# Optimization experiments

Measured on AMD Instinct MI355X. Metric: run time of the kernel, lower is better.

The kernel has to match this reference:

```python
import jax, jax.numpy as jnp
import numpy as np
from functools import partial


def deform_sample(inp, dy, dx):
    """Bilinear sample inp[b,c] at (y+dy[b,c,y,x], x+dx[b,c,y,x]) with zero padding.
    inp, dy, dx: [B, C, H, W] -> [B, C, H, W]. Matches torchvision deform_conv2d
    with 1x1 kernel and offset_groups == C (one offset pair per channel)."""
    B, C, H, W = inp.shape
    ys = jnp.arange(H, dtype=inp.dtype)[None, None, :, None] + dy  # [B,C,H,W]
    xs = jnp.arange(W, dtype=inp.dtype)[None, None, None, :] + dx
    y0f = jnp.floor(ys)
    x0f = jnp.floor(xs)
    wy = ys - y0f
    wx = xs - x0f
    y0 = y0f.astype(jnp.int32)
    x0 = x0f.astype(jnp.int32)
    flat = inp.reshape(B, C, H * W)

    def gather(yi, xi):
        valid = (yi >= 0) & (yi < H) & (xi >= 0) & (xi < W)
        idx = jnp.clip(yi, 0, H - 1) * W + jnp.clip(xi, 0, W - 1)
        v = jnp.take_along_axis(flat, idx.reshape(B, C, H * W), axis=2).reshape(B, C, H, W)
        return jnp.where(valid, v, jnp.zeros((), inp.dtype))

    return ((1 - wy) * (1 - wx) * gather(y0, x0)
            + (1 - wy) * wx * gather(y0, x0 + 1)
            + wy * (1 - wx) * gather(y0 + 1, x0)
            + wy * wx * gather(y0 + 1, x0 + 1))


def atm_layer(x, offset, w_weight, w_bias, h_weight, h_bias, local_weight, local_bias,
              fc1_w, fc1_b, fc2_w, fc2_b, proj_w, proj_b):
    B, H, W, C = x.shape
    x_nchw = jnp.transpose(x, (0, 3, 1, 2))  # [B,C,H,W]
    zeros = jnp.zeros_like(x_nchw)

    # ATM along w: offset[:, :C] is x-offset (offset_t[:,1::2]), y-offset 0
    sw = deform_sample(x_nchw, zeros, offset[:, :C])
    w = jnp.einsum('bchw,oc->bhwo', sw, w_weight) + w_bias  # [B,H,W,C]

    # ATM along h: offset[:, C:] is y-offset (offset_t[:,0::2]), x-offset 0
    sh = deform_sample(x_nchw, offset[:, C:], zeros)
    h = jnp.einsum('bchw,oc->bhwo', sh, h_weight) + h_bias

    # depthwise 5x5 conv, padding 2
    c = jax.lax.conv_general_dilated(
        x_nchw, local_weight, window_strides=(1, 1), padding=((2, 2), (2, 2)),
        feature_group_count=C, dimension_numbers=('NCHW', 'OIHW', 'NCHW'))
    c = jnp.transpose(c, (0, 2, 3, 1)) + local_bias  # [B,H,W,C]

    # gating MLP: global average -> fc1 -> GELU -> fc2 -> softmax over 3 branches
    a = (w + h + c).mean(axis=(1, 2))  # [B,C]
    a = jax.nn.gelu(a @ fc1_w.T + fc1_b, approximate=False)
    a = a @ fc2_w.T + fc2_b  # [B,3C]
    a = jnp.transpose(a.reshape(B, C, 3), (2, 0, 1))  # [3,B,C]
    a = jax.nn.softmax(a, axis=0)[:, :, None, None, :]  # [3,B,1,1,C]

    out = w * a[0] + h * a[1] + c * a[2]
    out = out @ proj_w.T + proj_b
    return out


def setup_inputs() -> dict:
    C = 256
    B, H, W = 16, 64, 64
    key = jax.random.key(0)
    ks = jax.random.split(key, 16)
    bnd = 1.0 / np.sqrt(C)
    hid = C // 4
    return {
        'x': jax.random.normal(ks[0], (B, H, W, C), jnp.float32),
        'offset': jax.random.normal(ks[1], (B, 2 * C, H, W), jnp.float32),
        'w_weight': jax.random.uniform(ks[2], (C, C), jnp.float32, -bnd, bnd),
        'w_bias': jax.random.uniform(ks[3], (C,), jnp.float32, -bnd, bnd),
        'h_weight': jax.random.uniform(ks[4], (C, C), jnp.float32, -bnd, bnd),
        'h_bias': jax.random.uniform(ks[5], (C,), jnp.float32, -bnd, bnd),
        'local_weight': jax.random.uniform(ks[6], (C, 1, 5, 5), jnp.float32, -0.2, 0.2),
        'local_bias': jax.random.uniform(ks[7], (C,), jnp.float32, -0.2, 0.2),
        'fc1_w': jax.random.uniform(ks[8], (hid, C), jnp.float32, -bnd, bnd),
        'fc1_b': jax.random.uniform(ks[9], (hid,), jnp.float32, -bnd, bnd),
        'fc2_w': jax.random.uniform(ks[10], (3 * C, hid), jnp.float32, -1.0 / np.sqrt(hid), 1.0 / np.sqrt(hid)),
        'fc2_b': jax.random.uniform(ks[11], (3 * C,), jnp.float32, -1.0 / np.sqrt(hid), 1.0 / np.sqrt(hid)),
        'proj_w': jax.random.uniform(ks[12], (C, C), jnp.float32, -bnd, bnd),
        'proj_b': jax.random.uniform(ks[13], (C,), jnp.float32, -bnd, bnd),
    }


def reference(x, offset, w_weight, w_bias, h_weight, h_bias, local_weight, local_bias,
              fc1_w, fc1_b, fc2_w, fc2_b, proj_w, proj_b):
    return atm_layer(x, offset, w_weight, w_bias, h_weight, h_bias, local_weight,
                     local_bias, fc1_w, fc1_b, fc2_w, fc2_b, proj_w, proj_b)
```

## Files before the change

kernel.cpp:

```cpp
#include <hip/hip_runtime.h>
#include <hip/hip_bf16.h>

typedef _Float16 half4_t __attribute__((ext_vector_type(4)));
typedef _Float16 half8 __attribute__((ext_vector_type(8)));
typedef float f32x4 __attribute__((ext_vector_type(4)));

#define BB 16
#define HH 64
#define WW2 64
#define CC 256

__global__ __launch_bounds__(256) void k_pre(
    const float* __restrict__ Ww, const float* __restrict__ Wh,
    const float* __restrict__ pw,
    _Float16* __restrict__ WwT, _Float16* __restrict__ WhT,
    _Float16* __restrict__ pf, float* __restrict__ sums)
{
  __shared__ _Float16 tile[64][65];
  const int blk = blockIdx.x;
  const int t = threadIdx.x;

  if (blk < 32) {
    const int nt = blk & 3, kt = (blk >> 2) & 3, mat = blk >> 4;
    const float* src = mat ? Wh : Ww;
    _Float16* dst = mat ? WhT : WwT;
    const int n0 = nt * 64, k0 = kt * 64;
    const int sl = t & 63;
    #pragma unroll
    for (int p = 0; p < 16; p++) {
      int chl = (t >> 6) + p * 4;
      tile[chl][sl] = (_Float16)src[(size_t)(n0 + chl) * 256 + k0 + sl];
    }
    __syncthreads();
    #pragma unroll
    for (int p = 0; p < 2; p++) {
      int pl = (t >> 3) + p * 32;
      int c8 = (t & 7) * 8;
      half8 hv;
      #pragma unroll
      for (int r = 0; r < 8; r++) hv[r] = tile[c8 + r][pl];
      *(half8*)(dst + (size_t)(k0 + pl) * 256 + n0 + c8) = hv;
    }
  } else if (blk < 80) {
    sums[(blk - 32) * 256 + t] = 0.f;
  } else {
    int i = (blk - 80) * 2048 + t * 8;
    float4 v0 = *(const float4*)(pw + i);
    float4 v1 = *(const float4*)(pw + i + 4);
    half8 h = {(_Float16)v0.x, (_Float16)v0.y, (_Float16)v0.z, (_Float16)v0.w,
               (_Float16)v1.x, (_Float16)v1.y, (_Float16)v1.z, (_Float16)v1.w};
    *(half8*)(pf + i) = h;
  }
}

__global__ __launch_bounds__(256) void k_transA(
    const float* __restrict__ x, const float* __restrict__ off,
    _Float16* __restrict__ swb, float* __restrict__ ssw)
{
  __shared__ _Float16 tile[64][65];
  __shared__ _Float16 xr[64][68];
  __shared__ float red[4][64];

  const int work = (blockIdx.x & 7) * 512 + (blockIdx.x >> 3);
  const int st   = work & 63;
  const int cht  = (work >> 6) & 3;
  const int b    = work >> 8;
  const int t = threadIdx.x;

  const int ch0 = cht * 64;
  const float* src = off + ((size_t)b * 512 + ch0) * 4096 + st * 64;
  const int sl = t & 63;
  #pragma unroll
  for (int p = 0; p < 16; p++) {
    int chl = (t >> 6) + p * 4;
    tile[chl][sl] = (_Float16)src[(size_t)chl * 4096 + sl];
  }

  const float* xs_src = x + ((size_t)(b * 64 + st) * 64) * 256 + ch0;
  const int xrow = t >> 2;
  const int c16 = (t & 3) * 16;
  #pragma unroll
  for (int j = 0; j < 4; j++) {
    float4 v = *(const float4*)(xs_src + (size_t)xrow * 256 + c16 + j * 4);
    half4_t h = {(_Float16)v.x, (_Float16)v.y, (_Float16)v.z, (_Float16)v.w};
    *(half4_t*)(&xr[xrow][c16 + j * 4]) = h;
  }
  __syncthreads();

  const int cl = t & 63, xg = t >> 6;
  const int cg = ch0 + cl;
  _Float16* sp = swb + ((size_t)(b * 64 + st) * 64) * 256 + cg;
  float asw = 0.f;
  #pragma unroll
  for (int k = 0; k < 16; k++) {
    int xi = xg * 16 + k;
    float dx = (float)tile[cl][xi];
    float xs2 = (float)xi + dx;
    float xf = floorf(xs2);
    float wx = xs2 - xf;
    int xq = (int)xf;
    float v0 = (xq >= 0 && xq < 64) ? (float)xr[xq][cl] : 0.f;
    float v1 = (xq + 1 >= 0 && xq + 1 < 64) ? (float)xr[xq + 1][cl] : 0.f;
    float swv = (1.f - wx) * v0 + wx * v1;
    sp[(size_t)xi * 256] = (_Float16)swv;
    asw += swv;
  }
  red[xg][cl] = asw;
  __syncthreads();
  if (t < 64)
    atomicAdd(&ssw[b * CC + ch0 + t],
              red[0][t] + red[1][t] + red[2][t] + red[3][t]);
}

__global__ __launch_bounds__(256) void k_transB(const float* __restrict__ off,
                                                _Float16* __restrict__ offBT)
{
  __shared__ _Float16 tile[64][65];
  const int work = (blockIdx.x & 7) * 512 + (blockIdx.x >> 3);
  const int st   = work & 63;
  const int cht  = (work >> 6) & 3;
  const int b    = work >> 8;
  const int t = threadIdx.x;

  const int ch0 = 256 + cht * 64;
  const float* src = off + ((size_t)b * 512 + ch0) * 4096 + st * 64;
  const int sl = t & 63;
  #pragma unroll
  for (int p = 0; p < 16; p++) {
    int chl = (t >> 6) + p * 4;
    tile[chl][sl] = (_Float16)src[(size_t)chl * 4096 + sl];
  }
  __syncthreads();

  #pragma unroll
  for (int p = 0; p < 2; p++) {
    int pl = (t >> 3) + p * 32;
    int c8 = (t & 7) * 8;
    half8 hv;
    #pragma unroll
    for (int r = 0; r < 8; r++) hv[r] = tile[c8 + r][pl];
    int s = st * 64 + pl;
    size_t pix = (size_t)b * 4096 + (s & 63) * 64 + (s >> 6);
    *(half8*)(offBT + pix * 256 + cht * 64 + c8) = hv;
  }
}

__global__ __launch_bounds__(256) void k_conv(
    const float* __restrict__ x, const float* __restrict__ lw,
    _Float16* __restrict__ cvb, float* __restrict__ scv)
{
  const int work = (blockIdx.x & 7) * 128 + (blockIdx.x >> 3);
  const int b = work >> 6, y = work & 63;
  const int c = threadIdx.x;

  float wgt[25];
  #pragma unroll
  for (int q = 0; q < 25; q++) wgt[q] = lw[c * 25 + q];

  const float* xb = x + (size_t)b * HH * WW2 * CC + c;
  const float* rp[5];
  bool yv[5];
  #pragma unroll
  for (int ky = 0; ky < 5; ky++) {
    int yy = y + ky - 2;
    yv[ky] = (yy >= 0 && yy < HH);
    rp[ky] = xb + (size_t)(yv[ky] ? yy : 0) * WW2 * CC;
  }

  _Float16* cp = cvb + ((size_t)b * 4096 + y * 64) * CC + c;
  float acc5[5] = {0.f, 0.f, 0.f, 0.f, 0.f};
  float acv = 0.f;

  #pragma unroll 5
  for (int u = 0; u < 70; ++u) {
    acc5[(u + 2) % 5] = 0.f;
    if (u < 64) {
      float c0 = yv[0] ? rp[0][u * CC] : 0.f;
      float c1 = yv[1] ? rp[1][u * CC] : 0.f;
      float c2 = yv[2] ? rp[2][u * CC] : 0.f;
      float c3 = yv[3] ? rp[3][u * CC] : 0.f;
      float c4 = yv[4] ? rp[4][u * CC] : 0.f;
      #pragma unroll
      for (int kx = 0; kx < 5; kx++) {
        acc5[(u + 7 - kx) % 5] += wgt[0 + kx] * c0 + wgt[5 + kx] * c1 +
                                  wgt[10 + kx] * c2 + wgt[15 + kx] * c3 +
                                  wgt[20 + kx] * c4;
      }
    }
    int xi = u - 2;
    if (xi >= 0 && xi < 64) {
      float cv = acc5[(u + 3) % 5];
      cp[(size_t)xi * CC] = (_Float16)cv;
      acv += cv;
    }
  }
  atomicAdd(&scv[b * CC + c], acv);
}

__global__ __launch_bounds__(256) void k_col(
    const float* __restrict__ x, const _Float16* __restrict__ offBT,
    _Float16* __restrict__ shb, float* __restrict__ ssh)
{
  __shared__ _Float16 xc[HH * CC];
  const int work = (blockIdx.x & 7) * 128 + (blockIdx.x >> 3);
  const int b = work >> 6, xi = work & 63;
  const int t = threadIdx.x;
  const int c = t;

  #pragma unroll
  for (int p = 0; p < 16; p++) {
    int yy = p * 4 + (t >> 6);
    int c4 = (t & 63) * 4;
    float4 v = *(const float4*)(x + ((size_t)(b * HH + yy) * WW2 + xi) * CC + c4);
    half4_t h = {(_Float16)v.x, (_Float16)v.y, (_Float16)v.z, (_Float16)v.w};
    *(half4_t*)(xc + yy * CC + c4) = h;
  }
  __syncthreads();

  const _Float16* obt = offBT + ((size_t)(b * WW2 + xi) * HH) * CC + c;
  _Float16* hp = shb + ((size_t)(b * HH) * WW2 + xi) * CC + c;
  float ash = 0.f;
  #pragma unroll 8
  for (int yy = 0; yy < 64; yy++) {
    float dy = (float)obt[(size_t)yy * CC];
    float ys = (float)yy + dy;
    float yf = floorf(ys);
    float wy = ys - yf;
    int yq = (int)yf;
    float u0 = (yq >= 0 && yq < HH) ? (float)xc[yq * CC + c] : 0.f;
    float u1 = (yq + 1 >= 0 && yq + 1 < HH) ? (float)xc[(yq + 1) * CC + c] : 0.f;
    float shv = (1.f - wy) * u0 + wy * u1;
    hp[(size_t)yy * WW2 * CC] = (_Float16)shv;
    ash += shv;
  }
  atomicAdd(&ssh[b * CC + c], ash);
}

__global__ __launch_bounds__(256) void k_gate(
    const float* __restrict__ ssw, const float* __restrict__ ssh, const float* __restrict__ scv,
    const float* __restrict__ Ww, const float* __restrict__ bw,
    const float* __restrict__ Wh, const float* __restrict__ bh,
    const float* __restrict__ blc,
    const float* __restrict__ fc1w, const float* __restrict__ fc1b,
    const float* __restrict__ fc2w, const float* __restrict__ fc2b,
    _Float16* __restrict__ gh, float* __restrict__ bcomb)
{
  __shared__ float sswl[CC], sshl[CC], avgl[CC], tl[64];
  const int b = blockIdx.x, tid = threadIdx.x;
  sswl[tid] = ssw[b * CC + tid];
  sshl[tid] = ssh[b * CC + tid];
  __syncthreads();

  float acc = scv[b * CC + tid];
  for (int c = 0; c < CC; c++)
    acc += sswl[c] * Ww[tid * CC + c] + sshl[c] * Wh[tid * CC + c];
  avgl[tid] = acc * (1.f / (HH * WW2)) + bw[tid] + bh[tid] + blc[tid];
  __syncthreads();

  if (tid < 64) {
    float a = fc1b[tid];
    for (int o = 0; o < CC; o++) a += avgl[o] * fc1w[tid * CC + o];
    tl[tid] = 0.5f * a * (1.f + erff(a * 0.70710678118654752f));
  }
  __syncthreads();

  float g[3];
  #pragma unroll
  for (int j = 0; j < 3; j++) {
    float a = fc2b[tid * 3 + j];
    for (int k = 0; k < 64; k++) a += tl[k] * fc2w[(tid * 3 + j) * 64 + k];
    g[j] = a;
  }
  float m = fmaxf(g[0], fmaxf(g[1], g[2]));
  float e0 = expf(g[0] - m), e1 = expf(g[1] - m), e2 = expf(g[2] - m);
  float inv = 1.f / (e0 + e1 + e2);
  float a0 = e0 * inv, a1 = e1 * inv, a2 = e2 * inv;
  gh[(0 * BB + b) * CC + tid] = (_Float16)a0;
  gh[(1 * BB + b) * CC + tid] = (_Float16)a1;
  gh[(2 * BB + b) * CC + tid] = (_Float16)a2;
  bcomb[b * CC + tid] = a0 * bw[tid] + a1 * bh[tid] + a2 * blc[tid];
}

__global__ __launch_bounds__(256) void k_mats(
    const _Float16* __restrict__ pf, const _Float16* __restrict__ gh,
    const _Float16* __restrict__ WwT, const _Float16* __restrict__ WhT,
    const float* __restrict__ bcomb, const float* __restrict__ pb,
    _Float16* __restrict__ Bcat, float* __restrict__ bias_out)
{
  const int blk = (blockIdx.x & 7) * 16 + (blockIdx.x >> 3);
  const int ob = blk & 3;
  const int br = (blk >> 2) & 1;
  const int b  = blk >> 3;
  const int o0 = ob * 64;
  const int tid = threadIdx.x;
  const int wid = tid >> 6, l = tid & 63;
  const int n0 = wid * 64;
  const int lr = l & 15;
  const int kg = (l >> 4) * 8;
  const int jr = (l >> 4) * 4;

  const _Float16* WT  = br ? WhT : WwT;
  const _Float16* ghb = gh + (size_t)(br * BB + b) * CC;

  f32x4 acc[4][4];
  #pragma unroll
  for (int mi = 0; mi < 4; mi++)
    #pragma unroll
    for (int ni = 0; ni < 4; ni++) acc[mi][ni] = (f32x4){0.f, 0.f, 0.f, 0.f};

  #pragma unroll
  for (int ks = 0; ks < 8; ks++) {
    half8 gv = *(const half8*)(ghb + kg + ks * 32);
    half8 a[4], bbv[4];
    #pragma unroll
    for (int mi = 0; mi < 4; mi++)
      a[mi] = *(const half8*)(pf + (size_t)(o0 + mi * 16 + lr) * CC + kg + ks * 32) * gv;
    #pragma unroll
    for (int ni = 0; ni < 4; ni++)
      bbv[ni] = *(const half8*)(WT + (size_t)(n0 + ni * 16 + lr) * CC + kg + ks * 32);
    #pragma unroll
    for (int mi = 0; mi < 4; mi++)
      #pragma unroll
      for (int ni = 0; ni < 4; ni++)
        acc[mi][ni] = __builtin_amdgcn_mfma_f32_16x16x32_f16(a[mi], bbv[ni], acc[mi][ni], 0, 0, 0);
  }

  #pragma unroll
  for (int ni = 0; ni < 4; ni++) {
    int kcol = n0 + ni * 16 + lr;
    #pragma unroll
    for (int mi = 0; mi < 4; mi++) {
      #pragma unroll
      for (int j = 0; j < 4; j++) {
        int o = o0 + mi * 16 + jr + j;
        Bcat[((size_t)b * CC + o) * 512 + br * 256 + kcol] = (_Float16)acc[mi][ni][j];
      }
    }
  }

  if (br == 0) {
    int o_l = tid >> 2, part = tid & 3;
    const _Float16* pr = pf + (size_t)(o0 + o_l) * CC + part * 64;
    const float* bc = bcomb + b * CC + part * 64;
    float s = 0.f;
    #pragma unroll
    for (int i = 0; i < 8; i++) {
      half8 h = *(const half8*)(pr + i * 8);
      #pragma unroll
      for (int r = 0; r < 8; r++) s += (float)h[r] * bc[i * 8 + r];
    }
    s += __shfl_xor(s, 1);
    s += __shfl_xor(s, 2);
    if (part == 0) bias_out[b * CC + o0 + o_l] = s + pb[o0 + o_l];
  }
}

#define APAD 264
__global__ __launch_bounds__(256) void k_gemm(
    const _Float16* __restrict__ swb, const _Float16* __restrict__ shb,
    const _Float16* __restrict__ cvb, const _Float16* __restrict__ Bcat,
    const _Float16* __restrict__ pf, const _Float16* __restrict__ a2h,
    const float* __restrict__ bias_out, float* __restrict__ out)
{
  __shared__ _Float16 smem[64 * APAD];

  const int work = (blockIdx.x & 7) * 128 + (blockIdx.x >> 3);
  const int r0 = work * 64;
  const int b = work >> 6;
  const int tid = threadIdx.x;
  const int wid = tid >> 6, l = tid & 63;
  const int n0 = wid * 64;
  const int lr = l & 15;
  const int kg = (l >> 4) * 8;
  const int jr = (l >> 4) * 4;

  const _Float16* bq = Bcat + ((size_t)b * CC + n0 + lr) * 512 + kg;

  f32x4 acc[4][4];
  #pragma unroll
  for (int mi = 0; mi < 4; mi++)
    #pragma unroll
    for (int ni = 0; ni < 4; ni++) acc[mi][ni] = (f32x4){0.f, 0.f, 0.f, 0.f};

  half8 st[8];
  {
    const _Float16* g = swb + (size_t)r0 * CC;
    #pragma unroll
    for (int p = 0; p < 8; p++) st[p] = *(const half8*)(g + p * 2048 + tid * 8);
    #pragma unroll
    for (int p = 0; p < 8; p++) {
      int i = p * 2048 + tid * 8;
      *(half8*)(smem + (i >> 8) * APAD + (i & 255)) = st[p];
    }
  }
  __syncthreads();
  {
    const _Float16* g = shb + (size_t)r0 * CC;
    #pragma unroll
    for (int p = 0; p < 8; p++) st[p] = *(const half8*)(g + p * 2048 + tid * 8);
  }
  #pragma unroll
  for (int ks = 0; ks < 8; ks++) {
    half8 a[4], bbv[4];
    #pragma unroll
    for (int mi = 0; mi < 4; mi++)
      a[mi] = *(const half8*)(smem + (mi * 16 + lr) * APAD + kg + ks * 32);
    #pragma unroll
    for (int ni = 0; ni < 4; ni++)
      bbv[ni] = *(const half8*)(bq + (size_t)ni * 16 * 512 + ks * 32);
    #pragma unroll
    for (int mi = 0; mi < 4; mi++)
      #pragma unroll
      for (int ni = 0; ni < 4; ni++)
        acc[mi][ni] = __builtin_amdgcn_mfma_f32_16x16x32_f16(a[mi], bbv[ni], acc[mi][ni], 0, 0, 0);
  }
  __syncthreads();
  #pragma unroll
  for (int p = 0; p < 8; p++) {
    int i = p * 2048 + tid * 8;
    *(half8*)(smem + (i >> 8) * APAD + (i & 255)) = st[p];
  }
  __syncthreads();
  {
    const _Float16* g = cvb + (size_t)r0 * CC;
    #pragma unroll
    for (int p = 0; p < 8; p++) st[p] = *(const half8*)(g + p * 2048 + tid * 8);
  }
  #pragma unroll
  for (int ks = 0; ks < 8; ks++) {
    half8 a[4], bbv[4];
    #pragma unroll
    for (int mi = 0; mi < 4; mi++)
      a[mi] = *(const half8*)(smem + (mi * 16 + lr) * APAD + kg + ks * 32);
    #pragma unroll
    for (int ni = 0; ni < 4; ni++)
      bbv[ni] = *(const half8*)(bq + (size_t)ni * 16 * 512 + 256 + ks * 32);
    #pragma unroll
    for (int mi = 0; mi < 4; mi++)
      #pragma unroll
      for (int ni = 0; ni < 4; ni++)
        acc[mi][ni] = __builtin_amdgcn_mfma_f32_16x16x32_f16(a[mi], bbv[ni], acc[mi][ni], 0, 0, 0);
  }
  __syncthreads();
  #pragma unroll
  for (int p = 0; p < 8; p++) {
    int i = p * 2048 + tid * 8;
    *(half8*)(smem + (i >> 8) * APAD + (i & 255)) = st[p];
  }
  __syncthreads();
  const _Float16* a2b = a2h + (size_t)b * CC;
  #pragma unroll
  for (int ks = 0; ks < 8; ks++) {
    half8 a2v = *(const half8*)(a2b + kg + ks * 32);
    half8 a[4], bbv[4];
    #pragma unroll
    for (int mi = 0; mi < 4; mi++)
      a[mi] = *(const half8*)(smem + (mi * 16 + lr) * APAD + kg + ks * 32);
    #pragma unroll
    for (int ni = 0; ni < 4; ni++)
      bbv[ni] = *(const half8*)(pf + (size_t)(n0 + ni * 16 + lr) * CC + kg + ks * 32) * a2v;
    #pragma unroll
    for (int mi = 0; mi < 4; mi++)
      #pragma unroll
      for (int ni = 0; ni < 4; ni++)
        acc[mi][ni] = __builtin_amdgcn_mfma_f32_16x16x32_f16(a[mi], bbv[ni], acc[mi][ni], 0, 0, 0);
  }

  #pragma unroll
  for (int ni = 0; ni < 4; ni++) {
    int col = n0 + ni * 16 + lr;
    float bo = bias_out[b * CC + col];
    #pragma unroll
    for (int mi = 0; mi < 4; mi++) {
      #pragma unroll
      for (int j = 0; j < 4; j++) {
        size_t idx = (size_t)(r0 + mi * 16 + jr + j) * CC + col;
        out[idx] = acc[mi][ni][j] + bo;
      }
    }
  }
}

extern "C" void kernel_launch(void* const* d_in, const int* in_sizes, int n_in,
                              void* d_out, int out_size, void* d_ws, size_t ws_size,
                              hipStream_t stream)
{
  const float* x    = (const float*)d_in[0];
  const float* off  = (const float*)d_in[1];
  const float* Ww   = (const float*)d_in[2];
  const float* bw   = (const float*)d_in[3];
  const float* Wh   = (const float*)d_in[4];
  const float* bh   = (const float*)d_in[5];
  const float* lw   = (const float*)d_in[6];
  const float* blc  = (const float*)d_in[7];
  const float* fc1w = (const float*)d_in[8];
  const float* fc1b = (const float*)d_in[9];
  const float* fc2w = (const float*)d_in[10];
  const float* fc2b = (const float*)d_in[11];
  const float* pw   = (const float*)d_in[12];
  const float* pb   = (const float*)d_in[13];
  float* out = (float*)d_out;

  char* ws = (char*)d_ws;
  _Float16* shb   = (_Float16*)(ws + 0);
  _Float16* cvb   = (_Float16*)(ws + 33554432);
  _Float16* offBT = (_Float16*)(ws + 67108864);
  _Float16* swb   = (_Float16*)(ws + 100663296);
  _Float16* Bcat  = (_Float16*)(ws + 134217728);
  _Float16* pf    = (_Float16*)(ws + 138412032);
  _Float16* gh    = (_Float16*)(ws + 138543104);
  float* bcomb    = (float*)(ws + 138567680);
  float* bias_out = (float*)(ws + 138584064);
  _Float16* WwT = (_Float16*)((char*)d_out + 0);
  _Float16* WhT = (_Float16*)((char*)d_out + 131072);
  float* sums   = (float*)((char*)d_out + 262144);
  float* ssw = sums, *ssh = sums + 4096, *scv = sums + 8192;

  k_pre<<<112, 256, 0, stream>>>(Ww, Wh, pw, WwT, WhT, pf, sums);
  k_transB<<<4096, 256, 0, stream>>>(off, offBT);
  k_col<<<BB * WW2, 256, 0, stream>>>(x, offBT, shb, ssh);
  k_transA<<<4096, 256, 0, stream>>>(x, off, swb, ssw);
  k_conv<<<BB * HH, 256, 0, stream>>>(x, lw, cvb, scv);
  k_gate<<<BB, 256, 0, stream>>>(ssw, ssh, scv, Ww, bw, Wh, bh, blc,
                                 fc1w, fc1b, fc2w, fc2b, gh, bcomb);
  k_mats<<<128, 256, 0, stream>>>(pf, gh, WwT, WhT, bcomb, pb, Bcat, bias_out);
  k_gemm<<<1024, 256, 0, stream>>>(swb, shb, cvb, Bcat, pf, gh + 2 * BB * CC,
                                   bias_out, out);
}
```

Baseline: 261.1 us.

## Split conv, column-sample and GEMM kernels into finer blocks for more parallelism

Doubles the grid for k_conv, k_col and k_gemm by halving each block's work. k_conv now splits each row into x-halves and computes 8 outputs per group from a 12-column register window instead of a rolling accumulator. k_col splits channels in half, so each block stages only 128 channels in LDS and two thread groups cover 32 rows each. k_gemm moves from 64-row to 32-row tiles. The aim is better occupancy and load balance across the CUs (1024 blocks is only a few waves). The cost is redundant halo loads in the conv, more atomics, and more reloads of the B matrix in the GEMM.

```diff
diff --git a/kernel.cpp b/kernel.cpp
--- a/kernel.cpp
+++ b/kernel.cpp
@@ -149,8 +149,10 @@
     const float* __restrict__ x, const float* __restrict__ lw,
     _Float16* __restrict__ cvb, float* __restrict__ scv)
 {
-  const int work = (blockIdx.x & 7) * 128 + (blockIdx.x >> 3);
-  const int b = work >> 6, y = work & 63;
+  const int work = (blockIdx.x & 7) * 256 + (blockIdx.x >> 3);
+  const int xh = work & 1;
+  const int y  = (work >> 1) & 63;
+  const int b  = work >> 7;
   const int c = threadIdx.x;
 
   float wgt[25];
@@ -168,29 +170,34 @@
   }
 
   _Float16* cp = cvb + ((size_t)b * 4096 + y * 64) * CC + c;
-  float acc5[5] = {0.f, 0.f, 0.f, 0.f, 0.f};
   float acv = 0.f;
-
-  #pragma unroll 5
-  for (int u = 0; u < 70; ++u) {
-    acc5[(u + 2) % 5] = 0.f;
-    if (u < 64) {
-      float c0 = yv[0] ? rp[0][u * CC] : 0.f;
-      float c1 = yv[1] ? rp[1][u * CC] : 0.f;
-      float c2 = yv[2] ? rp[2][u * CC] : 0.f;
-      float c3 = yv[3] ? rp[3][u * CC] : 0.f;
-      float c4 = yv[4] ? rp[4][u * CC] : 0.f;
+  const int x0 = xh * 32;
+
+  for (int g = 0; g < 4; ++g) {
+    const int u0 = x0 + g * 8;
+    float col[60];
+    #pragma unroll
+    for (int j = 0; j < 12; j++) {
+      int xx = u0 + j - 2;
+      bool xv = (xx >= 0 && xx < 64);
+      int xxc = xv ? xx : 0;
+      #pragma unroll
+      for (int ky = 0; ky < 5; ky++) {
+        float v = rp[ky][(size_t)xxc * CC];
+        col[j * 5 + ky] = (xv && yv[ky]) ? v : 0.f;
+      }
+    }
+    #pragma unroll
+    for (int o = 0; o < 8; o++) {
+      float cv = 0.f;
       #pragma unroll
       for (int kx = 0; kx < 5; kx++) {
-        acc5[(u + 7 - kx) % 5] += wgt[0 + kx] * c0 + wgt[5 + kx] * c1 +
-                                  wgt[10 + kx] * c2 + wgt[15 + kx] * c3 +
-                                  wgt[20 + kx] * c4;
+        const int j5 = (o + kx) * 5;
+        cv += wgt[0 + kx]  * col[j5 + 0] + wgt[5 + kx]  * col[j5 + 1] +
+              wgt[10 + kx] * col[j5 + 2] + wgt[15 + kx] * col[j5 + 3] +
+              wgt[20 + kx] * col[j5 + 4];
       }
-    }
-    int xi = u - 2;
-    if (xi >= 0 && xi < 64) {
-      float cv = acc5[(u + 3) % 5];
-      cp[(size_t)xi * CC] = (_Float16)cv;
+      cp[(size_t)(u0 + o) * CC] = (_Float16)cv;
       acv += cv;
     }
   }
@@ -201,39 +208,46 @@
     const float* __restrict__ x, const _Float16* __restrict__ offBT,
     _Float16* __restrict__ shb, float* __restrict__ ssh)
 {
-  __shared__ _Float16 xc[HH * CC];
-  const int work = (blockIdx.x & 7) * 128 + (blockIdx.x >> 3);
-  const int b = work >> 6, xi = work & 63;
+  __shared__ _Float16 xc[64 * 128];
+  const int work = (blockIdx.x & 7) * 256 + (blockIdx.x >> 3);
+  const int ch = work & 1;
+  const int xi = (work >> 1) & 63;
+  const int b  = work >> 7;
+  const int ch0 = ch * 128;
   const int t = threadIdx.x;
-  const int c = t;
-
-  #pragma unroll
-  for (int p = 0; p < 16; p++) {
-    int yy = p * 4 + (t >> 6);
-    int c4 = (t & 63) * 4;
-    float4 v = *(const float4*)(x + ((size_t)(b * HH + yy) * WW2 + xi) * CC + c4);
-    half4_t h = {(_Float16)v.x, (_Float16)v.y, (_Float16)v.z, (_Float16)v.w};
-    *(half4_t*)(xc + yy * CC + c4) = h;
-  }
-  __syncthreads();
-
-  const _Float16* obt = offBT + ((size_t)(b * WW2 + xi) * HH) * CC + c;
-  _Float16* hp = shb + ((size_t)(b * HH) * WW2 + xi) * CC + c;
+
+  #pragma unroll
+  for (int p = 0; p < 4; p++) {
+    int i = p * 2048 + t * 8;
+    int yy = i >> 7, cl = i & 127;
+    const float* s = x + ((size_t)(b * 64 + yy) * 64 + xi) * 256 + ch0 + cl;
+    float4 v0 = *(const float4*)(s);
+    float4 v1 = *(const float4*)(s + 4);
+    half8 h = {(_Float16)v0.x, (_Float16)v0.y, (_Float16)v0.z, (_Float16)v0.w,
+               (_Float16)v1.x, (_Float16)v1.y, (_Float16)v1.z, (_Float16)v1.w};
+    *(half8*)(xc + i) = h;
+  }
+  __syncthreads();
+
+  const int cl = t & 127, yg = t >> 7;
+  const _Float16* obt = offBT + ((size_t)(b * 64 + xi) * 64) * 256 + ch0 + cl;
+  _Float16* hp = shb + ((size_t)(b * 64) * 64 + xi) * 256 + ch0 + cl;
   float ash = 0.f;
   #pragma unroll 8
-  for (int yy = 0; yy < 64; yy++) {
-    float dy = (float)obt[(size_t)yy * CC];
+  for (int k = 0; k < 32; k++) {
+    int yy = yg * 32 + k;
+    float dy = (float)obt[(size_t)yy * 256];
     float ys = (float)yy + dy;
     float yf = floorf(ys);
     float wy = ys - yf;
     int yq = (int)yf;
-    float u0 = (yq >= 0 && yq < HH) ? (float)xc[yq * CC + c] : 0.f;
-    float u1 = (yq + 1 >= 0 && yq + 1 < HH) ? (float)xc[(yq + 1) * CC + c] : 0.f;
+    float u0 = (yq >= 0 && yq < 64) ? (float)xc[yq * 128 + cl] : 0.f;
+    float u1 = (yq + 1 >= 0 && yq + 1 < 64) ? (float)xc[(yq + 1) * 128 + cl] : 0.f;
     float shv = (1.f - wy) * u0 + wy * u1;
-    hp[(size_t)yy * WW2 * CC] = (_Float16)shv;
+    hp[(size_t)yy * 64 * 256] = (_Float16)shv;
     ash += shv;
   }
-  atomicAdd(&ssh[b * CC + c], ash);
+  atomicAdd(&ssh[b * CC + ch0 + cl], ash);
 }
 
 __global__ __launch_bounds__(256) void k_gate(
@@ -362,11 +376,11 @@
     const _Float16* __restrict__ pf, const _Float16* __restrict__ a2h,
     const float* __restrict__ bias_out, float* __restrict__ out)
 {
-  __shared__ _Float16 smem[64 * APAD];
-
-  const int work = (blockIdx.x & 7) * 128 + (blockIdx.x >> 3);
-  const int r0 = work * 64;
-  const int b = work >> 6;
+  __shared__ _Float16 smem[32 * APAD];
+
+  const int work = (blockIdx.x & 7) * 256 + (blockIdx.x >> 3);
+  const int r0 = work * 32;
+  const int b = work >> 7;
   const int tid = threadIdx.x;
   const int wid = tid >> 6, l = tid & 63;
   const int n0 = wid * 64;
@@ -376,19 +390,19 @@
 
   const _Float16* bq = Bcat + ((size_t)b * CC + n0 + lr) * 512 + kg;
 
-  f32x4 acc[4][4];
-  #pragma unroll
-  for (int mi = 0; mi < 4; mi++)
+  f32x4 acc[2][4];
+  #pragma unroll
+  for (int mi = 0; mi < 2; mi++)
     #pragma unroll
     for (int ni = 0; ni < 4; ni++) acc[mi][ni] = (f32x4){0.f, 0.f, 0.f, 0.f};
 
-  half8 st[8];
+  half8 st[4];
   {
     const _Float16* g = swb + (size_t)r0 * CC;
     #pragma unroll
-    for (int p = 0; p < 8; p++) st[p] = *(const half8*)(g + p * 2048 + tid * 8);
-    #pragma unroll
-    for (int p = 0; p < 8; p++) {
+    for (int p = 0; p < 4; p++) st[p] = *(const half8*)(g + p * 2048 + tid * 8);
+    #pragma unroll
+    for (int p = 0; p < 4; p++) {
       int i = p * 2048 + tid * 8;
       *(half8*)(smem + (i >> 8) * APAD + (i & 255)) = st[p];
     }
@@ -397,26 +411,26 @@
   {
     const _Float16* g = shb + (size_t)r0 * CC;
     #pragma unroll
-    for (int p = 0; p < 8; p++) st[p] = *(const half8*)(g + p * 2048 + tid * 8);
+    for (int p = 0; p < 4; p++) st[p] = *(const half8*)(g + p * 2048 + tid * 8);
   }
   #pragma unroll
   for (int ks = 0; ks < 8; ks++) {
-    half8 a[4], bbv[4];
-    #pragma unroll
-    for (int mi = 0; mi < 4; mi++)
+    half8 a[2], bbv[4];
+    #pragma unroll
+    for (int mi = 0; mi < 2; mi++)
       a[mi] = *(const half8*)(smem + (mi * 16 + lr) * APAD + kg + ks * 32);
     #pragma unroll
     for (int ni = 0; ni < 4; ni++)
       bbv[ni] = *(const half8*)(bq + (size_t)ni * 16 * 512 + ks * 32);
     #pragma unroll
-    for (int mi = 0; mi < 4; mi++)
+    for (int mi = 0; mi < 2; mi++)
       #pragma unroll
       for (int ni = 0; ni < 4; ni++)
         acc[mi][ni] = __builtin_amdgcn_mfma_f32_16x16x32_f16(a[mi], bbv[ni], acc[mi][ni], 0, 0, 0);
   }
   __syncthreads();
   #pragma unroll
-  for (int p = 0; p < 8; p++) {
+  for (int p = 0; p < 4; p++) {
     int i = p * 2048 + tid * 8;
     *(half8*)(smem + (i >> 8) * APAD + (i & 255)) = st[p];
   }
@@ -424,26 +438,26 @@
   {
     const _Float16* g = cvb + (size_t)r0 * CC;
     #pragma unroll
-    for (int p = 0; p < 8; p++) st[p] = *(const half8*)(g + p * 2048 + tid * 8);
+    for (int p = 0; p < 4; p++) st[p] = *(const half8*)(g + p * 2048 + tid * 8);
   }
   #pragma unroll
   for (int ks = 0; ks < 8; ks++) {
-    half8 a[4], bbv[4];
-    #pragma unroll
-    for (int mi = 0; mi < 4; mi++)
+    half8 a[2], bbv[4];
+    #pragma unroll
+    for (int mi = 0; mi < 2; mi++)
       a[mi] = *(const half8*)(smem + (mi * 16 + lr) * APAD + kg + ks * 32);
     #pragma unroll
     for (int ni = 0; ni < 4; ni++)
       bbv[ni] = *(const half8*)(bq + (size_t)ni * 16 * 512 + 256 + ks * 32);
     #pragma unroll
-    for (int mi = 0; mi < 4; mi++)
+    for (int mi = 0; mi < 2; mi++)
       #pragma unroll
       for (int ni = 0; ni < 4; ni++)
         acc[mi][ni] = __builtin_amdgcn_mfma_f32_16x16x32_f16(a[mi], bbv[ni], acc[mi][ni], 0, 0, 0);
   }
   __syncthreads();
   #pragma unroll
-  for (int p = 0; p < 8; p++) {
+  for (int p = 0; p < 4; p++) {
     int i = p * 2048 + tid * 8;
     *(half8*)(smem + (i >> 8) * APAD + (i & 255)) = st[p];
   }
@@ -452,15 +466,15 @@
   #pragma unroll
   for (int ks = 0; ks < 8; ks++) {
     half8 a2v = *(const half8*)(a2b + kg + ks * 32);
-    half8 a[4], bbv[4];
-    #pragma unroll
-    for (int mi = 0; mi < 4; mi++)
+    half8 a[2], bbv[4];
+    #pragma unroll
+    for (int mi = 0; mi < 2; mi++)
       a[mi] = *(const half8*)(smem + (mi * 16 + lr) * APAD + kg + ks * 32);
     #pragma unroll
     for (int ni = 0; ni < 4; ni++)
       bbv[ni] = *(const half8*)(pf + (size_t)(n0 + ni * 16 + lr) * CC + kg + ks * 32) * a2v;
     #pragma unroll
-    for (int mi = 0; mi < 4; mi++)
+    for (int mi = 0; mi < 2; mi++)
       #pragma unroll
       for (int ni = 0; ni < 4; ni++)
         acc[mi][ni] = __builtin_amdgcn_mfma_f32_16x16x32_f16(a[mi], bbv[ni], acc[mi][ni], 0, 0, 0);
@@ -471,7 +485,7 @@
     int col = n0 + ni * 16 + lr;
     float bo = bias_out[b * CC + col];
     #pragma unroll
-    for (int mi = 0; mi < 4; mi++) {
+    for (int mi = 0; mi < 2; mi++) {
       #pragma unroll
       for (int j = 0; j < 4; j++) {
         size_t idx = (size_t)(r0 + mi * 16 + jr + j) * CC + col;
@@ -518,12 +532,12 @@
 
   k_pre<<<112, 256, 0, stream>>>(Ww, Wh, pw, WwT, WhT, pf, sums);
   k_transB<<<4096, 256, 0, stream>>>(off, offBT);
-  k_col<<<BB * WW2, 256, 0, stream>>>(x, offBT, shb, ssh);
+  k_col<<<2048, 256, 0, stream>>>(x, offBT, shb, ssh);
   k_transA<<<4096, 256, 0, stream>>>(x, off, swb, ssw);
-  k_conv<<<BB * HH, 256, 0, stream>>>(x, lw, cvb, scv);
+  k_conv<<<2048, 256, 0, stream>>>(x, lw, cvb, scv);
   k_gate<<<BB, 256, 0, stream>>>(ssw, ssh, scv, Ww, bw, Wh, bh, blc,
                                  fc1w, fc1b, fc2w, fc2b, gh, bcomb);
   k_mats<<<128, 256, 0, stream>>>(pf, gh, WwT, WhT, bcomb, pb, Bcat, bias_out);
-  k_gemm<<<1024, 256, 0, stream>>>(swb, shb, cvb, Bcat, pf, gh + 2 * BB * CC,
+  k_gemm<<<2048, 256, 0, stream>>>(swb, shb, cvb, Bcat, pf, gh + 2 * BB * CC,
                                    bias_out, out);
 }
```

Measured after the change: 285.4 us. +9.3%, slower.
